# Kernel tuning notes

Measured on AMD Instinct MI355X. Metric: run time of the kernel, lower is better.

## Reference

```python
import jax, jax.numpy as jnp
import numpy as np

N, H, O, E = 32768, 512, 512, 16


def setup_inputs() -> dict:
    key = jax.random.key(0)
    k0, k1, k2 = jax.random.split(key, 3)
    x = jax.random.normal(k0, (N, H), dtype=jnp.float32)
    # gate Linear(H -> E)
    Wg = jax.random.normal(k1, (E, H), dtype=jnp.float32) * (1.0 / np.sqrt(H))
    bg = jnp.zeros((E,), dtype=jnp.float32)
    # expert Linears(H -> O), stacked [E, O, H]
    We = jax.random.normal(k2, (E, O, H), dtype=jnp.float32) * (1.0 / np.sqrt(H))
    be = jnp.zeros((E, O), dtype=jnp.float32)
    return {"x": x, "Wg": Wg, "bg": bg, "We": We, "be": be}


def reference(x, Wg, bg, We, be):
    # gate: softmax over experts, then top-1 (argmax)
    logits = x @ Wg.T + bg                       # [N, E]
    weights = jax.nn.softmax(logits, axis=-1)
    expert_idx = jnp.argmax(weights, axis=-1)    # [N]
    # run every expert on every token, then select the top-1 expert's output.
    # (note: original module does NOT scale output by the gate weight)
    all_out = jnp.einsum('nh,eoh->neo', x, We) + be[None]   # [N, E, O]
    out = jnp.take_along_axis(all_out, expert_idx[:, None, None], axis=1)[:, 0]  # [N, O]
    return out
```

## Files before the change

### kernel.cpp

```cpp
#include <hip/hip_runtime.h>
#include <hip/hip_bf16.h>
#include <stdint.h>

#define NTOK 32768
#define HDIM 512
#define ODIM 512
#define NEXP 16

#define TM 128
#define TN 128
#define BK 64
#define MTILES 32

#define CSTRIDE 32

typedef __bf16 bf16x8 __attribute__((ext_vector_type(8)));
typedef float  floatx4 __attribute__((ext_vector_type(4)));

__device__ __forceinline__ unsigned pk2(unsigned lo, unsigned hi) {
  return (lo >> 16) | (hi & 0xffff0000u);
}

__device__ __forceinline__ bf16x8 asbf8(uint4 u) { bf16x8 v; __builtin_memcpy(&v, &u, 16); return v; }

__device__ __forceinline__ void split3(float4 a, float4 b, uint4* H, uint4* M, uint4* L) {
  float f[8] = {a.x, a.y, a.z, a.w, b.x, b.y, b.z, b.w};
  unsigned h[8], m[8], l[8];
#pragma unroll
  for (int j = 0; j < 8; ++j) {
    union { float F; unsigned U; } u; u.F = f[j];
    h[j] = u.U & 0xffff0000u;
    union { unsigned U; float F; } hv; hv.U = h[j];
    float r1 = f[j] - hv.F;
    union { float F; unsigned U; } r1u; r1u.F = r1;
    m[j] = r1u.U & 0xffff0000u;
    union { unsigned U; float F; } mv; mv.U = m[j];
    float r2 = r1 - mv.F;
    union { float F; unsigned U; } r2u; r2u.F = r2;
    l[j] = r2u.U;
  }
  H->x = pk2(h[0], h[1]); H->y = pk2(h[2], h[3]); H->z = pk2(h[4], h[5]); H->w = pk2(h[6], h[7]);
  M->x = pk2(m[0], m[1]); M->y = pk2(m[2], m[3]); M->z = pk2(m[4], m[5]); M->w = pk2(m[6], m[7]);
  L->x = pk2(l[0], l[1]); L->y = pk2(l[2], l[3]); L->z = pk2(l[4], l[5]); L->w = pk2(l[6], l[7]);
}

#define GLDS16(g, l) __builtin_amdgcn_global_load_lds( \
    (const __attribute__((address_space(1))) unsigned int*)(g), \
    (__attribute__((address_space(3))) unsigned int*)(l), 16, 0, 0)

__global__ __launch_bounds__(256) void cvt_we_kernel(const float* __restrict__ We,
                                                     unsigned short* __restrict__ out) {
  int i = blockIdx.x * 256 + threadIdx.x;
  const float4* src = (const float4*)We;
  float4 a = src[2 * i];
  float4 b = src[2 * i + 1];
  union { float F; unsigned U; } t[8] = {{a.x},{a.y},{a.z},{a.w},{b.x},{b.y},{b.z},{b.w}};
  uint4 o;
  o.x = pk2(t[0].U, t[1].U); o.y = pk2(t[2].U, t[3].U);
  o.z = pk2(t[4].U, t[5].U); o.w = pk2(t[6].U, t[7].U);
  ((uint4*)out)[i] = o;
}

__global__ __launch_bounds__(256) void gate_kernel(const float* __restrict__ x,
                                                   const float* __restrict__ Wg,
                                                   const float* __restrict__ bg,
                                                   int* __restrict__ counts,
                                                   int* __restrict__ buckets,
                                                   unsigned short* __restrict__ xbf) {
  __shared__ __align__(16) unsigned short whf[16][64][8];
  __shared__ __align__(16) unsigned short wmf[16][64][8];
  __shared__ __align__(16) unsigned short wlf[16][64][8];
  __shared__ __align__(16) float red[4][4][16][20];

  int t = threadIdx.x;
  int lane = t & 63;
  int w = t >> 6;
  int tok0 = blockIdx.x * 64;

#pragma unroll
  for (int q = 0; q < 4; ++q) {
    int id = q * 256 + t;
    int s = id >> 6;
    int l = id & 63;
    const float* src = Wg + (size_t)(l & 15) * HDIM + s * 32 + (l >> 4) * 8;
    float4 a = *(const float4*)src;
    float4 b = *(const float4*)(src + 4);
    uint4 H, M, L;
    split3(a, b, &H, &M, &L);
    *(uint4*)&whf[s][l][0] = H;
    *(uint4*)&wmf[s][l][0] = M;
    *(uint4*)&wlf[s][l][0] = L;
  }
  __syncthreads();

  int fr = lane & 15;
  int quad = lane >> 4;
  floatx4 acc[4] = {};

#pragma unroll
  for (int si = 0; si < 4; ++si) {
    int s = w * 4 + si;
    bf16x8 bh = *(const bf16x8*)&whf[s][lane][0];
    bf16x8 bm = *(const bf16x8*)&wmf[s][lane][0];
    bf16x8 bl = *(const bf16x8*)&wlf[s][lane][0];
#pragma unroll
    for (int mt = 0; mt < 4; ++mt) {
      size_t row = tok0 + mt * 16 + fr;
      const float* xp = x + row * HDIM + s * 32 + quad * 8;
      float4 a = *(const float4*)xp;
      float4 b = *(const float4*)(xp + 4);
      uint4 H, M, L;
      split3(a, b, &H, &M, &L);
      *(uint4*)(xbf + row * HDIM + s * 32 + quad * 8) = H;
      bf16x8 ah = asbf8(H), am = asbf8(M), al = asbf8(L);
      acc[mt] = __builtin_amdgcn_mfma_f32_16x16x32_bf16(ah, bh, acc[mt], 0, 0, 0);
      acc[mt] = __builtin_amdgcn_mfma_f32_16x16x32_bf16(ah, bm, acc[mt], 0, 0, 0);
      acc[mt] = __builtin_amdgcn_mfma_f32_16x16x32_bf16(am, bh, acc[mt], 0, 0, 0);
      acc[mt] = __builtin_amdgcn_mfma_f32_16x16x32_bf16(am, bm, acc[mt], 0, 0, 0);
      acc[mt] = __builtin_amdgcn_mfma_f32_16x16x32_bf16(ah, bl, acc[mt], 0, 0, 0);
      acc[mt] = __builtin_amdgcn_mfma_f32_16x16x32_bf16(al, bh, acc[mt], 0, 0, 0);
      acc[mt] = __builtin_amdgcn_mfma_f32_16x16x32_bf16(am, bl, acc[mt], 0, 0, 0);
      acc[mt] = __builtin_amdgcn_mfma_f32_16x16x32_bf16(al, bm, acc[mt], 0, 0, 0);
    }
  }

#pragma unroll
  for (int mt = 0; mt < 4; ++mt)
#pragma unroll
    for (int i = 0; i < 4; ++i)
      red[w][mt][quad * 4 + i][fr] = acc[mt][i];
  __syncthreads();

  if (t < 64) {
    int tk = t;
    int mt = tk >> 4;
    int r = tk & 15;
    float4 tot4[4];
#pragma unroll
    for (int eq = 0; eq < 4; ++eq) tot4[eq] = *(const float4*)&bg[eq * 4];
#pragma unroll
    for (int ww = 0; ww < 4; ++ww)
#pragma unroll
      for (int eq = 0; eq < 4; ++eq) {
        float4 v = *(const float4*)&red[ww][mt][r][eq * 4];
        tot4[eq].x += v.x; tot4[eq].y += v.y; tot4[eq].z += v.z; tot4[eq].w += v.w;
      }
    float tot[16];
#pragma unroll
    for (int eq = 0; eq < 4; ++eq) {
      tot[eq * 4 + 0] = tot4[eq].x; tot[eq * 4 + 1] = tot4[eq].y;
      tot[eq * 4 + 2] = tot4[eq].z; tot[eq * 4 + 3] = tot4[eq].w;
    }
    float bv = tot[0]; int bi = 0;
#pragma unroll
    for (int e = 1; e < NEXP; ++e) if (tot[e] > bv) { bv = tot[e]; bi = e; }

    int token = tok0 + tk;
    for (int ee = 0; ee < NEXP; ++ee) {
      int e = (ee + blockIdx.x) & 15;
      unsigned long long mask = __ballot(bi == e);
      if (mask) {
        int leader = __builtin_ctzll(mask);
        int base = 0;
        if (lane == leader) base = atomicAdd(&counts[e << 5], (int)__popcll(mask));
        base = __shfl(base, leader, 64);
        if (bi == e) {
          int rank = (int)__popcll(mask & ((1ull << lane) - 1ull));
          buckets[e * NTOK + base + rank] = token;
        }
      }
    }
  }
}

__global__ __launch_bounds__(256) void moe_gemm(const unsigned short* __restrict__ xbf,
                                                const unsigned short* __restrict__ webf,
                                                const float* __restrict__ be,
                                                const int* __restrict__ counts,
                                                const int* __restrict__ buckets,
                                                float* __restrict__ out) {
  int e = blockIdx.z;
  int cnt = counts[e << 5];
  int m0 = blockIdx.x * TM;
  if (m0 >= cnt) return;
  int o0 = blockIdx.y * TN;

  __shared__ __align__(16) unsigned short As[TM * BK];
  __shared__ __align__(16) unsigned short Bs[TN * BK];
  __shared__ int toks[TM];

  int t = threadIdx.x;
  int lane = t & 63;
  int w = t >> 6;

  if (t < TM) {
    int r = m0 + t;
    toks[t] = (r < cnt) ? buckets[e * NTOK + r] : buckets[e * NTOK];
  }
  __syncthreads();

  int lrow = lane >> 3;
  int sig = lane & 7;
  int c = sig ^ lrow;
  const unsigned short* agp[4];
  const unsigned short* bgp[4];
#pragma unroll
  for (int i = 0; i < 4; ++i) {
    int row = w * 32 + i * 8 + lrow;
    agp[i] = xbf + (size_t)toks[row] * HDIM + c * 8;
    bgp[i] = webf + ((size_t)e * ODIM + o0 + row) * HDIM + c * 8;
  }

  int wm = (w & 1) * 64;
  int wn = (w >> 1) * 64;
  int fr = lane & 15;
  int quad = lane >> 4;
  int mconst[4], m7[4], nconst[4], n7[4];
#pragma unroll
  for (int mt = 0; mt < 4; ++mt) {
    int m = wm + mt * 16 + fr;
    mconst[mt] = (m >> 3) * 512 + (m & 7) * 64;
    m7[mt] = m & 7;
    int n = wn + mt * 16 + fr;
    nconst[mt] = (n >> 3) * 512 + (n & 7) * 64;
    n7[mt] = n & 7;
  }

  floatx4 acc[4][4] = {};

  for (int k0 = 0; k0 < HDIM; k0 += BK) {
    __syncthreads();
#pragma unroll
    for (int i = 0; i < 4; ++i) {
      GLDS16(agp[i] + k0, As + (w * 4 + i) * 512);
      GLDS16(bgp[i] + k0, Bs + (w * 4 + i) * 512);
    }
    __syncthreads();

#pragma unroll
    for (int kk = 0; kk < 2; ++kk) {
      int cb = kk * 4 + quad;
      bf16x8 af[4], bf[4];
#pragma unroll
      for (int mt = 0; mt < 4; ++mt)
        af[mt] = *(const bf16x8*)(As + mconst[mt] + ((cb ^ m7[mt]) << 3));
#pragma unroll
      for (int nt = 0; nt < 4; ++nt)
        bf[nt] = *(const bf16x8*)(Bs + nconst[nt] + ((cb ^ n7[nt]) << 3));
#pragma unroll
      for (int mt = 0; mt < 4; ++mt)
#pragma unroll
        for (int nt = 0; nt < 4; ++nt)
          acc[mt][nt] = __builtin_amdgcn_mfma_f32_16x16x32_bf16(af[mt], bf[nt], acc[mt][nt], 0, 0, 0);
    }
  }

  int rbase = wm + quad * 4;
#pragma unroll
  for (int nt = 0; nt < 4; ++nt) {
    int col = o0 + wn + nt * 16 + fr;
    float bias = be[e * ODIM + col];
#pragma unroll
    for (int mt = 0; mt < 4; ++mt) {
#pragma unroll
      for (int i = 0; i < 4; ++i) {
        int rl = rbase + mt * 16 + i;
        if (m0 + rl < cnt) {
          out[(size_t)toks[rl] * ODIM + col] = acc[mt][nt][i] + bias;
        }
      }
    }
  }
}

#define WS_BUCKETS 4096
#define WS_XBF (WS_BUCKETS + NEXP * NTOK * 4)
#define WS_WEBF (WS_XBF + NTOK * HDIM * 2)

extern "C" void kernel_launch(void* const* d_in, const int* in_sizes, int n_in,
                              void* d_out, int out_size, void* d_ws, size_t ws_size,
                              hipStream_t stream) {
  const float* x  = (const float*)d_in[0];
  const float* Wg = (const float*)d_in[1];
  const float* bg = (const float*)d_in[2];
  const float* We = (const float*)d_in[3];
  const float* be = (const float*)d_in[4];
  float* out = (float*)d_out;
  char* ws = (char*)d_ws;

  int* counts = (int*)ws;
  int* buckets = (int*)(ws + WS_BUCKETS);
  unsigned short* xbf  = (unsigned short*)(ws + WS_XBF);
  unsigned short* webf = (unsigned short*)(ws + WS_WEBF);

  hipMemsetAsync(counts, 0, NEXP * CSTRIDE * 4, stream);
  cvt_we_kernel<<<NEXP * ODIM * HDIM / 8 / 256, 256, 0, stream>>>(We, webf);
  gate_kernel<<<NTOK / 64, 256, 0, stream>>>(x, Wg, bg, counts, buckets, xbf);
  moe_gemm<<<dim3(MTILES, ODIM / TN, NEXP), 256, 0, stream>>>(xbf, webf, be, counts, buckets, out);
}
```

Before: 224.9 us.

## Double-buffer LDS tiles in MoE GEMM and prefetch x in gate kernel

The expert GEMM now uses two LDS buffers per operand. The async global-to-LDS loads for the next K-slice are issued before the MFMAs on the current slice, which removes one barrier per iteration and overlaps load latency with compute. The gate kernel preloads the next 32-column slice of x into registers while the current slice is split and multiplied. Both kernels get a launch-bounds occupancy hint of 2, and the bias load is hoisted out of the epilogue. The costs are twice the LDS per GEMM block and more registers in both kernels, which may limit occupancy.

```diff
diff --git a/kernel.cpp b/kernel.cpp
--- a/kernel.cpp
+++ b/kernel.cpp
@@ -61,12 +61,12 @@
   ((uint4*)out)[i] = o;
 }
 
-__global__ __launch_bounds__(256) void gate_kernel(const float* __restrict__ x,
-                                                   const float* __restrict__ Wg,
-                                                   const float* __restrict__ bg,
-                                                   int* __restrict__ counts,
-                                                   int* __restrict__ buckets,
-                                                   unsigned short* __restrict__ xbf) {
+__global__ __launch_bounds__(256, 2) void gate_kernel(const float* __restrict__ x,
+                                                      const float* __restrict__ Wg,
+                                                      const float* __restrict__ bg,
+                                                      int* __restrict__ counts,
+                                                      int* __restrict__ buckets,
+                                                      unsigned short* __restrict__ xbf) {
   __shared__ __align__(16) unsigned short whf[16][64][8];
   __shared__ __align__(16) unsigned short wmf[16][64][8];
   __shared__ __align__(16) unsigned short wlf[16][64][8];
@@ -97,20 +97,37 @@
   int quad = lane >> 4;
   floatx4 acc[4] = {};
 
+  const float* xbase[4];
+#pragma unroll
+  for (int mt = 0; mt < 4; ++mt)
+    xbase[mt] = x + (size_t)(tok0 + mt * 16 + fr) * HDIM + (w * 4) * 32 + quad * 8;
+
+  float4 xa[4], xb[4];
+#pragma unroll
+  for (int mt = 0; mt < 4; ++mt) {
+    xa[mt] = *(const float4*)(xbase[mt]);
+    xb[mt] = *(const float4*)(xbase[mt] + 4);
+  }
+
 #pragma unroll
   for (int si = 0; si < 4; ++si) {
     int s = w * 4 + si;
     bf16x8 bh = *(const bf16x8*)&whf[s][lane][0];
     bf16x8 bm = *(const bf16x8*)&wmf[s][lane][0];
     bf16x8 bl = *(const bf16x8*)&wlf[s][lane][0];
+    float4 na[4], nb[4];
+    if (si < 3) {
+#pragma unroll
+      for (int mt = 0; mt < 4; ++mt) {
+        na[mt] = *(const float4*)(xbase[mt] + (si + 1) * 32);
+        nb[mt] = *(const float4*)(xbase[mt] + (si + 1) * 32 + 4);
+      }
+    }
 #pragma unroll
     for (int mt = 0; mt < 4; ++mt) {
       size_t row = tok0 + mt * 16 + fr;
-      const float* xp = x + row * HDIM + s * 32 + quad * 8;
-      float4 a = *(const float4*)xp;
-      float4 b = *(const float4*)(xp + 4);
       uint4 H, M, L;
-      split3(a, b, &H, &M, &L);
+      split3(xa[mt], xb[mt], &H, &M, &L);
       *(uint4*)(xbf + row * HDIM + s * 32 + quad * 8) = H;
       bf16x8 ah = asbf8(H), am = asbf8(M), al = asbf8(L);
       acc[mt] = __builtin_amdgcn_mfma_f32_16x16x32_bf16(ah, bh, acc[mt], 0, 0, 0);
@@ -121,6 +138,10 @@
       acc[mt] = __builtin_amdgcn_mfma_f32_16x16x32_bf16(al, bh, acc[mt], 0, 0, 0);
       acc[mt] = __builtin_amdgcn_mfma_f32_16x16x32_bf16(am, bl, acc[mt], 0, 0, 0);
       acc[mt] = __builtin_amdgcn_mfma_f32_16x16x32_bf16(al, bm, acc[mt], 0, 0, 0);
+    }
+    if (si < 3) {
+#pragma unroll
+      for (int mt = 0; mt < 4; ++mt) { xa[mt] = na[mt]; xb[mt] = nb[mt]; }
     }
   }
 
@@ -173,20 +194,20 @@
   }
 }
 
-__global__ __launch_bounds__(256) void moe_gemm(const unsigned short* __restrict__ xbf,
-                                                const unsigned short* __restrict__ webf,
-                                                const float* __restrict__ be,
-                                                const int* __restrict__ counts,
-                                                const int* __restrict__ buckets,
-                                                float* __restrict__ out) {
+__global__ __launch_bounds__(256, 2) void moe_gemm(const unsigned short* __restrict__ xbf,
+                                                   const unsigned short* __restrict__ webf,
+                                                   const float* __restrict__ be,
+                                                   const int* __restrict__ counts,
+                                                   const int* __restrict__ buckets,
+                                                   float* __restrict__ out) {
   int e = blockIdx.z;
   int cnt = counts[e << 5];
   int m0 = blockIdx.x * TM;
   if (m0 >= cnt) return;
   int o0 = blockIdx.y * TN;
 
-  __shared__ __align__(16) unsigned short As[TM * BK];
-  __shared__ __align__(16) unsigned short Bs[TN * BK];
+  __shared__ __align__(16) unsigned short As[2][TM * BK];
+  __shared__ __align__(16) unsigned short Bs[2][TN * BK];
   __shared__ int toks[TM];
 
   int t = threadIdx.x;
@@ -226,16 +247,30 @@
     n7[mt] = n & 7;
   }
 
+  float bias[4];
+#pragma unroll
+  for (int nt = 0; nt < 4; ++nt)
+    bias[nt] = be[e * ODIM + o0 + wn + nt * 16 + fr];
+
   floatx4 acc[4][4] = {};
 
-  for (int k0 = 0; k0 < HDIM; k0 += BK) {
+#pragma unroll
+  for (int i = 0; i < 4; ++i) {
+    GLDS16(agp[i], As[0] + (w * 4 + i) * 512);
+    GLDS16(bgp[i], Bs[0] + (w * 4 + i) * 512);
+  }
+
+  for (int k = 0; k < HDIM / BK; ++k) {
+    int p = k & 1;
     __syncthreads();
-#pragma unroll
-    for (int i = 0; i < 4; ++i) {
-      GLDS16(agp[i] + k0, As + (w * 4 + i) * 512);
-      GLDS16(bgp[i] + k0, Bs + (w * 4 + i) * 512);
-    }
-    __syncthreads();
+    if (k < HDIM / BK - 1) {
+      int koff = (k + 1) * BK;
+#pragma unroll
+      for (int i = 0; i < 4; ++i) {
+        GLDS16(agp[i] + koff, As[1 - p] + (w * 4 + i) * 512);
+        GLDS16(bgp[i] + koff, Bs[1 - p] + (w * 4 + i) * 512);
+      }
+    }
 
 #pragma unroll
     for (int kk = 0; kk < 2; ++kk) {
@@ -243,10 +278,10 @@
       bf16x8 af[4], bf[4];
 #pragma unroll
       for (int mt = 0; mt < 4; ++mt)
-        af[mt] = *(const bf16x8*)(As + mconst[mt] + ((cb ^ m7[mt]) << 3));
+        af[mt] = *(const bf16x8*)(As[p] + mconst[mt] + ((cb ^ m7[mt]) << 3));
 #pragma unroll
       for (int nt = 0; nt < 4; ++nt)
-        bf[nt] = *(const bf16x8*)(Bs + nconst[nt] + ((cb ^ n7[nt]) << 3));
+        bf[nt] = *(const bf16x8*)(Bs[p] + nconst[nt] + ((cb ^ n7[nt]) << 3));
 #pragma unroll
       for (int mt = 0; mt < 4; ++mt)
 #pragma unroll
@@ -259,14 +294,13 @@
 #pragma unroll
   for (int nt = 0; nt < 4; ++nt) {
     int col = o0 + wn + nt * 16 + fr;
-    float bias = be[e * ODIM + col];
 #pragma unroll
     for (int mt = 0; mt < 4; ++mt) {
 #pragma unroll
       for (int i = 0; i < 4; ++i) {
         int rl = rbase + mt * 16 + i;
         if (m0 + rl < cnt) {
-          out[(size_t)toks[rl] * ODIM + col] = acc[mt][nt][i] + bias;
+          out[(size_t)toks[rl] * ODIM + col] = acc[mt][nt][i] + bias[nt];
         }
       }
     }
```

After: 209.4 us. 6.9% less time.
